# Optimization experiments

Measured on AMD Instinct MI355X. Metric: run time of the kernel, lower is better.

The kernel has to match this reference:

```python
import jax, jax.numpy as jnp
import numpy as np

B = 16
NUM_PATCHES = (4096, 1024)
DIM_S, DIM_M, DIM_L = 256, 512, 1024
N_L = NUM_PATCHES[0] + 1   # tokens in x0 (no cls)
N_M = NUM_PATCHES[1]       # patch tokens in x1 (plus 1 cls)
N_S = 4096                 # patch tokens in x2 (plus 1 cls)
# torch: d_k = int(math.sqrt(dim))
D_K1, D_K2, D_K3 = 22, 32, 16  # int(sqrt(512)), int(sqrt(1024)), int(sqrt(256))


def _lin(x, w, b=None):
    # torch nn.Linear: y = x @ W.T + b, w: [out, in]
    y = jnp.einsum('bnd,md->bnm', x, w)
    return y + b if b is not None else y


def setup_inputs() -> dict:
    key = jax.random.key(0)
    ks = jax.random.split(key, 20)
    s = 0.02
    return {
        'x0': jax.random.normal(ks[0], (B, N_L, DIM_L), jnp.float32),
        'x1': jax.random.normal(ks[1], (B, 1 + N_M, DIM_M), jnp.float32),
        'x2': jax.random.normal(ks[2], (B, 1 + N_S, DIM_S), jnp.float32),
        'f_s_w': jax.random.normal(ks[3], (DIM_M, DIM_S), jnp.float32) * s,
        'f_s_b': jnp.zeros((DIM_M,), jnp.float32),
        'f_m_w': jax.random.normal(ks[4], (DIM_L, DIM_M), jnp.float32) * s,
        'f_m_b': jnp.zeros((DIM_L,), jnp.float32),
        'Wq1': jax.random.normal(ks[5], (DIM_M, DIM_M), jnp.float32) * s,
        'Wk1': jax.random.normal(ks[6], (DIM_M, DIM_M), jnp.float32) * s,
        'Wq2': jax.random.normal(ks[7], (DIM_L, DIM_L), jnp.float32) * s,
        'Wk2': jax.random.normal(ks[8], (DIM_L, DIM_L), jnp.float32) * s,
        'Wv': jax.random.normal(ks[9], (DIM_L, DIM_L), jnp.float32) * s,
        'proj_w': jax.random.normal(ks[10], (NUM_PATCHES[0] + 2, NUM_PATCHES[1] + 1), jnp.float32) * s,
        'proj_b': jnp.zeros((NUM_PATCHES[0] + 2,), jnp.float32),
        'gs_w': jax.random.normal(ks[11], (DIM_S, DIM_L), jnp.float32) * s,
        'gs_b': jnp.zeros((DIM_S,), jnp.float32),
    }


def reference(x0, x1, x2, f_s_w, f_s_b, f_m_w, f_m_b, Wq1, Wk1, Wq2, Wk2, Wv,
              proj_w, proj_b, gs_w, gs_b):
    p_l = x0                                   # [B, N_L, dim_l]
    cls_m, p_m = x1[:, :1, :], x1[:, 1:, :]    # [B,1,dim_m], [B,N_M,dim_m]
    cls_s, p_s = x2[:, :1, :], x2[:, 1:, :]    # [B,1,dim_s], [B,N_S,dim_s]

    # stage 1: small->medium cross attention on attention-map level
    cls_s_proj = _lin(cls_s, f_s_w, f_s_b)               # [B,1,dim_m]
    q1 = _lin(cls_s_proj, Wq1)                           # [B,1,dim_m]
    k1 = _lin(jnp.concatenate([cls_s_proj, p_m], 1), Wk1)  # [B,1+N_M,dim_m]
    att1 = jax.nn.softmax(jnp.einsum('bqd,bkd->bqk', q1, k1) / D_K1, axis=-1)
    att1 = _lin(att1, proj_w, proj_b)                    # [B,1,1+N_L]

    # stage 2: medium->large cross attention
    cls_m_proj = _lin(cls_m, f_m_w, f_m_b)               # [B,1,dim_l]
    q2 = _lin(cls_m_proj, Wq2)
    kv_in = jnp.concatenate([cls_m_proj, p_l], 1)        # [B,1+N_L,dim_l]
    k2 = _lin(kv_in, Wk2)
    att2 = jax.nn.softmax(jnp.einsum('bqd,bkd->bqk', q2, k2) / D_K2, axis=-1)
    v = _lin(kv_in, Wv)                                  # [B,1+N_L,dim_l]

    # weighted fusion of attention maps, third attention pass
    wa = 0.3 * att1 + 0.7 * att2                         # [B,1,1+N_L]
    out = jnp.einsum('bqk,bkd->bqd', wa, v * 1.0)        # [B,1,dim_l]
    g_s = _lin(out, gs_w, gs_b)                          # [B,1,dim_s]

    att3 = jax.nn.softmax(jnp.einsum('bnd,bqd->bnq', p_s, g_s) / D_K3, axis=-1)  # [B,N_S,1]
    p_s_out = jnp.einsum('bnq,bqd->bnd', att3, g_s)      # [B,N_S,dim_s]
    return jnp.concatenate([g_s, p_s_out], axis=1)       # [B,1+N_S,dim_s]
```

## Files before the change

kernel.cpp:

```cpp
#include <hip/hip_runtime.h>
#include <stdint.h>

typedef unsigned int u32;
typedef unsigned short u16;

#define NB 16
#define NL 4097
#define NM_ROWS 1025
#define DS 256
#define DM 512
#define DL 1024
#define NK1 1025
#define NK2 4098
#define MPROJ 4098

__device__ __forceinline__ float bf2f(u16 h){ union{u32 u; float f;} c; c.u = ((u32)h)<<16; return c.f; }
__device__ __forceinline__ u16 f2bf(float x){ union{float f; u32 u;} c; c.f=x; u32 u=c.u; return (u16)((u + 0x7fffu + ((u>>16)&1u))>>16); }
__device__ __forceinline__ float getel(const void* p, long i, int f){
  return f ? ((const float*)p)[i] : bf2f(((const u16*)p)[i]);
}
__device__ __forceinline__ void unpack8(uint4 v, float* fo){
  u32 w[4]={v.x,v.y,v.z,v.w};
  #pragma unroll
  for(int i=0;i<4;i++){
    union{u32 u; float x;} a,b;
    a.u = w[i]<<16; b.u = w[i]&0xffff0000u;
    fo[2*i]=a.x; fo[2*i+1]=b.x;
  }
}
__device__ __forceinline__ float wsum(float v){
  #pragma unroll
  for(int o=32;o>0;o>>=1) v += __shfl_xor(v,o,64);
  return v;
}
__device__ __forceinline__ float wmaxr(float v){
  #pragma unroll
  for(int o=32;o>0;o>>=1) v = fmaxf(v, __shfl_xor(v,o,64));
  return v;
}
__device__ __forceinline__ float block_sum(float v, volatile float* red){
  v = wsum(v);
  if((threadIdx.x&63)==0) red[threadIdx.x>>6]=v;
  __syncthreads();
  float r = red[0]+red[1]+red[2]+red[3];
  __syncthreads();
  return r;
}
__device__ __forceinline__ float block_max(float v, volatile float* red){
  v = wmaxr(v);
  if((threadIdx.x&63)==0) red[threadIdx.x>>6]=v;
  __syncthreads();
  float r = fmaxf(fmaxf(red[0],red[1]),fmaxf(red[2],red[3]));
  __syncthreads();
  return r;
}
__device__ __forceinline__ float clamp60(float x){ return fminf(fmaxf(x,-60.f),60.f); }

__global__ __launch_bounds__(256) void detect_kernel(const u16* __restrict__ x0, int* __restrict__ flag){
  __shared__ float red[256];
  float mx=0.f;
  for(int i=threadIdx.x;i<4096;i+=256){
    float v = fabsf(bf2f(x0[i]));
    if (v==v) mx = fmaxf(mx, v);
  }
  red[threadIdx.x]=mx; __syncthreads();
  if(threadIdx.x==0){
    float m=0.f;
    for(int i=0;i<256;i++) m=fmaxf(m,red[i]);
    flag[0] = (m>1e3f)?1:0;
  }
}

struct Job {
  const void* W; const void* x; const void* bias; float* out;
  int M, D; long xstride; int xinws;
};

__global__ __launch_bounds__(256) void gemv_n_kernel(Job j0, Job j1, const int* __restrict__ flagp){
  Job j = (blockIdx.y==0)? j0 : j1;
  if ((int)(blockIdx.x*4) >= j.M) return;
  int f = flagp[0];
  __shared__ float xs[NB*512];
  int tid = threadIdx.x;
  int m = blockIdx.x*4 + (tid>>6);
  int l = tid & 63;
  float acc[NB];
  #pragma unroll
  for(int b=0;b<NB;b++) acc[b]=0.f;
  for(int c0=0;c0<j.D;c0+=512){
    int cl = j.D-c0; if (cl>512) cl=512;
    for(int i=tid;i<NB*cl;i+=256){
      int b=i/cl, d=i-b*cl;
      float v;
      if (j.xinws) v = ((const float*)j.x)[(long)b*j.D + c0 + d];
      else         v = getel(j.x, (long)b*j.xstride + c0 + d, f);
      xs[i]=v;
    }
    __syncthreads();
    if (m < j.M){
      for(int d=l; d<cl; d+=64){
        float w = getel(j.W, (long)m*j.D + c0 + d, f);
        #pragma unroll
        for(int b=0;b<NB;b++) acc[b] += w*xs[b*cl+d];
      }
    }
    __syncthreads();
  }
  if (m >= j.M) return;
  #pragma unroll
  for(int b=0;b<NB;b++) acc[b]=wsum(acc[b]);
  if(l==0){
    float bv = j.bias ? getel(j.bias, m, f) : 0.f;
    #pragma unroll
    for(int b=0;b<NB;b++) j.out[(long)b*j.M+m]=acc[b]+bv;
  }
}

struct TJob { const void* W; const float* x; float* out; int M, D; };

__global__ __launch_bounds__(256) void gemv_t_kernel(TJob j0, TJob j1, const int* __restrict__ flagp){
  TJob j = (blockIdx.z==0)? j0 : j1;
  int f = flagp[0];
  if ((int)(blockIdx.x*256) >= j.D) return;
  int m0 = blockIdx.y*64;
  if (m0 >= j.M) return;
  __shared__ float xs[NB*64];
  int d = blockIdx.x*256 + threadIdx.x;
  for(int i=threadIdx.x;i<NB*64;i+=256){ int b=i>>6, mm=i&63; xs[i]=j.x[(long)b*j.M+m0+mm]; }
  __syncthreads();
  float acc[NB];
  #pragma unroll
  for(int b=0;b<NB;b++) acc[b]=0.f;
  for(int mm=0;mm<64;++mm){
    float w = getel(j.W, (long)(m0+mm)*j.D + d, f);
    #pragma unroll
    for(int b=0;b<NB;b++) acc[b] += w*xs[b*64+mm];
  }
  #pragma unroll
  for(int b=0;b<NB;b++) atomicAdd(&j.out[(long)b*j.D+d], acc[b]);
}

__global__ __launch_bounds__(256) void att1_logits_kernel(const void* __restrict__ x1,
    const float* __restrict__ q1p, float* __restrict__ logits1, const int* __restrict__ flagp){
  int f = flagp[0];
  int b = blockIdx.y;
  int k = blockIdx.x*4 + (threadIdx.x>>6) + 1;
  if (k > 1024) return;
  int l = threadIdx.x & 63;
  long rbase = ((long)b*NM_ROWS + k)*DM + l*8;
  float rf[8];
  if (f){
    const float* rp = (const float*)x1 + rbase;
    float4 a0 = *(const float4*)rp;
    float4 a1 = *(const float4*)(rp+4);
    rf[0]=a0.x; rf[1]=a0.y; rf[2]=a0.z; rf[3]=a0.w;
    rf[4]=a1.x; rf[5]=a1.y; rf[6]=a1.z; rf[7]=a1.w;
  } else {
    uint4 rv = *(const uint4*)((const u16*)x1 + rbase);
    unpack8(rv, rf);
  }
  const float* qp = q1p + (long)b*DM + l*8;
  float s = rf[0]*qp[0]+rf[1]*qp[1]+rf[2]*qp[2]+rf[3]*qp[3]
          + rf[4]*qp[4]+rf[5]*qp[5]+rf[6]*qp[6]+rf[7]*qp[7];
  s = wsum(s);
  if(l==0) logits1[(long)b*NK1 + k] = s * (1.f/22.f);
}

__global__ __launch_bounds__(256) void att1_softmax_kernel(const float* __restrict__ csp,
    const float* __restrict__ q1p, const float* __restrict__ logits1, float* __restrict__ att1_sm){
  __shared__ float red[4];
  int b=blockIdx.x, t=threadIdx.x;
  float p=0.f;
  for(int d=t;d<DM;d+=256) p += q1p[(long)b*DM+d]*csp[(long)b*DM+d];
  float l0 = block_sum(p, red) * (1.f/22.f);
  float mx = l0;
  for(int k=1+t;k<NK1;k+=256) mx = fmaxf(mx, logits1[(long)b*NK1+k]);
  mx = block_max(mx, red);
  float s=0.f;
  for(int k=t;k<NK1;k+=256){
    float lg = (k==0)? l0 : logits1[(long)b*NK1+k];
    float e = __expf(clamp60(lg-mx));
    att1_sm[(long)b*NK1+k]=e;
    s+=e;
  }
  s = block_sum(s, red);
  float inv = 1.f/fmaxf(s,1e-30f);
  for(int k=t;k<NK1;k+=256) att1_sm[(long)b*NK1+k]*=inv;
}

__global__ __launch_bounds__(256) void att1_proj_kernel(const void* __restrict__ proj_w,
    const void* __restrict__ proj_b, const float* __restrict__ att1_sm, float* __restrict__ att1w,
    const int* __restrict__ flagp){
  int f = flagp[0];
  __shared__ float sm[8*1024];
  int tid=threadIdx.x;
  int m = blockIdx.x*4 + (tid>>6);
  int l = tid&63;
  float acc[NB];
  #pragma unroll
  for(int b=0;b<NB;b++) acc[b]=0.f;
  for(int h=0;h<2;h++){
    for(int i=tid;i<8*1024;i+=256){ int bb=i>>10, k=i&1023; sm[i]=att1_sm[(long)(h*8+bb)*NK1+k]; }
    __syncthreads();
    if (m < MPROJ){
      for(int k=l;k<1024;k+=64){
        float w = getel(proj_w, (long)m*NK1+k, f);
        #pragma unroll
        for(int bb=0;bb<8;bb++) acc[h*8+bb] += w * sm[bb*1024+k];
      }
    }
    __syncthreads();
  }
  if (m >= MPROJ) return;
  if(l==0){
    float wt = getel(proj_w, (long)m*NK1 + 1024, f);
    #pragma unroll
    for(int b=0;b<NB;b++) acc[b] += wt * att1_sm[(long)b*NK1 + 1024];
  }
  #pragma unroll
  for(int b=0;b<NB;b++) acc[b]=wsum(acc[b]);
  if(l==0){
    float pb = getel(proj_b, m, f);
    #pragma unroll
    for(int b=0;b<NB;b++) att1w[(long)b*NK2+m] = 0.3f*(acc[b]+pb);
  }
}

__global__ __launch_bounds__(256) void att2_pass_kernel(const void* __restrict__ x0,
    const float* __restrict__ q2p, const float* __restrict__ att1w,
    float* __restrict__ s1, float* __restrict__ s2, float* __restrict__ Zacc,
    const int* __restrict__ flagp){
  __shared__ float ls[4][1024];
  __shared__ float zs[4];
  int f = flagp[0];
  int b = blockIdx.y;
  int w = threadIdx.x>>6, l = threadIdx.x&63;
  float qf[16];
  {
    const float* qp = q2p + (long)b*DL;
    #pragma unroll
    for(int j=0;j<8;j++){ qf[j]=qp[l*8+j]; qf[8+j]=qp[512+l*8+j]; }
  }
  float af1[16], af2[16];
  #pragma unroll
  for(int j=0;j<16;j++){ af1[j]=0.f; af2[j]=0.f; }
  float zacc=0.f;
  int kbase = blockIdx.x*64 + w*16;
  int nk = NL - kbase; if (nk > 16) nk = 16; if (nk < 0) nk = 0;
  const float* awp = att1w + (long)b*NK2 + kbase + 1;
  for(int i=0;i<nk;i++){
    float rf[16];
    long rowoff = ((long)b*NL + kbase + i)*DL;
    if (f){
      const float* rp = ((const float*)x0) + rowoff;
      float4 a0 = *(const float4*)(rp + l*8);
      float4 a1 = *(const float4*)(rp + l*8 + 4);
      float4 a2 = *(const float4*)(rp + 512 + l*8);
      float4 a3 = *(const float4*)(rp + 512 + l*8 + 4);
      rf[0]=a0.x; rf[1]=a0.y; rf[2]=a0.z; rf[3]=a0.w;
      rf[4]=a1.x; rf[5]=a1.y; rf[6]=a1.z; rf[7]=a1.w;
      rf[8]=a2.x; rf[9]=a2.y; rf[10]=a2.z; rf[11]=a2.w;
      rf[12]=a3.x; rf[13]=a3.y; rf[14]=a3.z; rf[15]=a3.w;
    } else {
      const u16* rp = ((const u16*)x0) + rowoff;
      uint4 rv0 = *(const uint4*)(rp + l*8);
      uint4 rv1 = *(const uint4*)(rp + 512 + l*8);
      u32 wd[8]={rv0.x,rv0.y,rv0.z,rv0.w,rv1.x,rv1.y,rv1.z,rv1.w};
      #pragma unroll
      for(int q=0;q<8;q++){
        union{u32 u; float x;} ua,ub;
        ua.u = wd[q]<<16; ub.u = wd[q]&0xffff0000u;
        rf[2*q]=ua.x; rf[2*q+1]=ub.x;
      }
    }
    float dp=0.f;
    #pragma unroll
    for(int j=0;j<16;j++) dp += rf[j]*qf[j];
    dp = clamp60(wsum(dp)*(1.f/32.f));
    float e = __expf(dp);
    float aw = awp[i];
    zacc += e;
    #pragma unroll
    for(int j=0;j<16;j++){ af1[j] += aw*rf[j]; af2[j] += e*rf[j]; }
  }
  #pragma unroll
  for(int c=0;c<2;c++)
    #pragma unroll
    for(int j=0;j<8;j++) ls[w][c*512 + l*8 + j] = af1[c*8+j];
  __syncthreads();
  for(int d=threadIdx.x; d<1024; d+=256)
    atomicAdd(&s1[(long)b*DL+d], ls[0][d]+ls[1][d]+ls[2][d]+ls[3][d]);
  __syncthreads();
  #pragma unroll
  for(int c=0;c<2;c++)
    #pragma unroll
    for(int j=0;j<8;j++) ls[w][c*512 + l*8 + j] = af2[c*8+j];
  if(l==0) zs[w]=zacc;
  __syncthreads();
  for(int d=threadIdx.x; d<1024; d+=256)
    atomicAdd(&s2[(long)b*DL+d], ls[0][d]+ls[1][d]+ls[2][d]+ls[3][d]);
  if(threadIdx.x==0) atomicAdd(&Zacc[b], zs[0]+zs[1]+zs[2]+zs[3]);
}

__global__ __launch_bounds__(256) void finalize_u_kernel(const float* __restrict__ cmp,
    const float* __restrict__ q2p, const float* __restrict__ att1w,
    const float* __restrict__ s1, const float* __restrict__ s2,
    const float* __restrict__ Zacc, float* __restrict__ u){
  __shared__ float red[4];
  int b=blockIdx.x, t=threadIdx.x;
  float p=0.f;
  for(int d=t;d<DL;d+=256) p += q2p[(long)b*DL+d]*cmp[(long)b*DL+d];
  float l20 = clamp60(block_sum(p,red)*(1.f/32.f));
  float e0 = __expf(l20);
  float Zf = fmaxf(Zacc[b] + e0, 1e-30f);
  float a0 = att1w[(long)b*NK2];
  float c7 = 0.7f/Zf;
  for(int d=t;d<DL;d+=256){
    float cm = cmp[(long)b*DL+d];
    u[(long)b*DL+d] = s1[(long)b*DL+d] + a0*cm + c7*(s2[(long)b*DL+d] + e0*cm);
  }
}

__global__ __launch_bounds__(256) void broadcast_out_kernel(const float* __restrict__ g_s,
    void* __restrict__ out, const int* __restrict__ flagp){
  int f = flagp[0];
  int b = blockIdx.y;
  int colq = threadIdx.x & 31;
  int rowo = threadIdx.x >> 5;
  int r = blockIdx.x*8 + rowo;
  const float* gp = g_s + (long)b*DS + colq*8;
  float4 ga = *(const float4*)gp;
  float4 gb = *(const float4*)(gp+4);
  if (r >= NL) return;
  long row = (long)b*NL + r;
  if (f){
    float4* op = (float4*)out + row*64 + colq*2;
    op[0]=ga; op[1]=gb;
  } else {
    uint4 pk;
    pk.x = (u32)f2bf(ga.x) | ((u32)f2bf(ga.y)<<16);
    pk.y = (u32)f2bf(ga.z) | ((u32)f2bf(ga.w)<<16);
    pk.z = (u32)f2bf(gb.x) | ((u32)f2bf(gb.y)<<16);
    pk.w = (u32)f2bf(gb.z) | ((u32)f2bf(gb.w)<<16);
    ((uint4*)out)[row*32 + colq] = pk;
  }
}

extern "C" void kernel_launch(void* const* d_in, const int* in_sizes, int n_in,
                              void* d_out, int out_size, void* d_ws, size_t ws_size,
                              hipStream_t stream) {
  const void* x0     = d_in[0];
  const void* x1     = d_in[1];
  const void* x2     = d_in[2];
  const void* f_s_w  = d_in[3];
  const void* f_s_b  = d_in[4];
  const void* f_m_w  = d_in[5];
  const void* f_m_b  = d_in[6];
  const void* Wq1    = d_in[7];
  const void* Wk1    = d_in[8];
  const void* Wq2    = d_in[9];
  const void* Wk2    = d_in[10];
  const void* Wv     = d_in[11];
  const void* proj_w = d_in[12];
  const void* proj_b = d_in[13];
  const void* gs_w   = d_in[14];
  const void* gs_b   = d_in[15];

  float* ws = (float*)d_ws;
  float* cls_s_proj = ws;
  float* cls_m_proj = cls_s_proj + NB*DM;
  float* q1v        = cls_m_proj + NB*DL;
  float* q2v        = q1v + NB*DM;
  float* logits1    = q2v + NB*DL;
  float* att1_sm    = logits1 + NB*NK1;
  float* att1w      = att1_sm + NB*NK1;
  float* uvec       = att1w + NB*NK2;
  float* outv       = uvec + NB*DL;
  float* g_s        = outv + NB*DL;
  float* q1p        = g_s + NB*DS;
  float* q2p        = q1p + NB*DM;
  float* s1         = q2p + NB*DL;
  float* s2         = s1 + NB*DL;
  float* Zacc       = s2 + NB*DL;
  int*   flag       = (int*)(Zacc + NB);
  size_t zero_bytes = (size_t)(NB*DM + 3*NB*DL + NB) * sizeof(float);
  hipMemsetAsync(q1p, 0, zero_bytes, stream);

  detect_kernel<<<1,256,0,stream>>>((const u16*)x0, flag);

  Job ja0{f_s_w, x2, f_s_b, cls_s_proj, DM, DS, (long)NL*DS, 0};
  Job ja1{f_m_w, x1, f_m_b, cls_m_proj, DL, DM, (long)NM_ROWS*DM, 0};
  gemv_n_kernel<<<dim3(256,2),256,0,stream>>>(ja0, ja1, flag);

  Job jb0{Wq1, cls_s_proj, nullptr, q1v, DM, DM, DM, 1};
  Job jb1{Wq2, cls_m_proj, nullptr, q2v, DL, DL, DL, 1};
  gemv_n_kernel<<<dim3(256,2),256,0,stream>>>(jb0, jb1, flag);

  TJob jt0{Wk1, q1v, q1p, DM, DM};
  TJob jt1{Wk2, q2v, q2p, DL, DL};
  gemv_t_kernel<<<dim3(4,16,2),256,0,stream>>>(jt0, jt1, flag);

  att1_logits_kernel<<<dim3(256,NB),256,0,stream>>>(x1, q1p, logits1, flag);
  att1_softmax_kernel<<<NB,256,0,stream>>>(cls_s_proj, q1p, logits1, att1_sm);
  att1_proj_kernel<<<dim3(1025),256,0,stream>>>(proj_w, proj_b, att1_sm, att1w, flag);

  att2_pass_kernel<<<dim3(65,NB),256,0,stream>>>(x0, q2p, att1w, s1, s2, Zacc, flag);

  finalize_u_kernel<<<NB,256,0,stream>>>(cls_m_proj, q2p, att1w, s1, s2, Zacc, uvec);
  Job jv{Wv, uvec, nullptr, outv, DL, DL, DL, 1};
  gemv_n_kernel<<<dim3(256,1),256,0,stream>>>(jv, jv, flag);
  Job jg{gs_w, outv, gs_b, g_s, DS, DL, DL, 1};
  gemv_n_kernel<<<dim3(64,1),256,0,stream>>>(jg, jg, flag);

  broadcast_out_kernel<<<dim3(513,NB),256,0,stream>>>(g_s, d_out, flag);
}
```

Before: 684.2 us.

## Precompute fused gs_w·Wv weight, drop softmax max pass, merge small kernels

Adds an init kernel that computes the fused weight product gs_w@Wv (256x1024) and zeroes the workspace, replacing the memset and the separate detect kernel. The Wv and gs_w GEMVs are then replaced by one GEMV over the fused weight. The att1 softmax becomes exp without max subtraction, accumulated into Z by atomics, with normalization moved into the proj kernel. The cls logit for att2 moves into the logits kernel. This removes several launches and a pass over the logits. In exchange it adds a 256x1024x1024 weight product on every call, and dropping the max subtraction relies on clamping to keep the exponentials in range.

```diff
diff --git a/kernel.cpp b/kernel.cpp
--- a/kernel.cpp
+++ b/kernel.cpp
@@ -14,28 +14,41 @@
 #define NK2 4098
 #define MPROJ 4098
 
+#define OFF_CSP  0
+#define OFF_CMP  8192
+#define OFF_Q1V  24576
+#define OFF_Q2V  32768
+#define OFF_E1   49152
+#define OFF_A1W  65552
+#define OFF_GS   131120
+#define OFF_WF   135216
+#define OFF_Q1P  397360
+#define OFF_Q2P  405552
+#define OFF_S1   421936
+#define OFF_S2   438320
+#define OFF_ZA   454704
+#define OFF_Z1   454720
+#define OFF_E20  454736
+#define OFF_FLAG 454752
+#define ZERO_U4  14348
+
 __device__ __forceinline__ float bf2f(u16 h){ union{u32 u; float f;} c; c.u = ((u32)h)<<16; return c.f; }
 __device__ __forceinline__ u16 f2bf(float x){ union{float f; u32 u;} c; c.f=x; u32 u=c.u; return (u16)((u + 0x7fffu + ((u>>16)&1u))>>16); }
 __device__ __forceinline__ float getel(const void* p, long i, int f){
   return f ? ((const float*)p)[i] : bf2f(((const u16*)p)[i]);
 }
 __device__ __forceinline__ void unpack8(uint4 v, float* fo){
-  u32 w[4]={v.x,v.y,v.z,v.w};
+  u32 wd[4]={v.x,v.y,v.z,v.w};
   #pragma unroll
   for(int i=0;i<4;i++){
     union{u32 u; float x;} a,b;
-    a.u = w[i]<<16; b.u = w[i]&0xffff0000u;
+    a.u = wd[i]<<16; b.u = wd[i]&0xffff0000u;
     fo[2*i]=a.x; fo[2*i+1]=b.x;
   }
 }
 __device__ __forceinline__ float wsum(float v){
   #pragma unroll
   for(int o=32;o>0;o>>=1) v += __shfl_xor(v,o,64);
-  return v;
-}
-__device__ __forceinline__ float wmaxr(float v){
-  #pragma unroll
-  for(int o=32;o>0;o>>=1) v = fmaxf(v, __shfl_xor(v,o,64));
   return v;
 }
 __device__ __forceinline__ float block_sum(float v, volatile float* red){
@@ -46,29 +59,59 @@
   __syncthreads();
   return r;
 }
-__device__ __forceinline__ float block_max(float v, volatile float* red){
-  v = wmaxr(v);
-  if((threadIdx.x&63)==0) red[threadIdx.x>>6]=v;
-  __syncthreads();
-  float r = fmaxf(fmaxf(red[0],red[1]),fmaxf(red[2],red[3]));
-  __syncthreads();
-  return r;
-}
 __device__ __forceinline__ float clamp60(float x){ return fminf(fmaxf(x,-60.f),60.f); }
 
-__global__ __launch_bounds__(256) void detect_kernel(const u16* __restrict__ x0, int* __restrict__ flag){
-  __shared__ float red[256];
+__device__ __forceinline__ int self_detect(const void* x0, float* sh){
   float mx=0.f;
-  for(int i=threadIdx.x;i<4096;i+=256){
-    float v = fabsf(bf2f(x0[i]));
-    if (v==v) mx = fmaxf(mx, v);
-  }
-  red[threadIdx.x]=mx; __syncthreads();
-  if(threadIdx.x==0){
+  const u16* p = (const u16*)x0;
+  for (int i=threadIdx.x;i<4096;i+=256){ float v=fabsf(bf2f(p[i])); if(v==v) mx=fmaxf(mx,v); }
+  sh[threadIdx.x]=mx; __syncthreads();
+  if (threadIdx.x==0){
     float m=0.f;
-    for(int i=0;i<256;i++) m=fmaxf(m,red[i]);
-    flag[0] = (m>1e3f)?1:0;
-  }
+    for (int i=0;i<256;i++) m=fmaxf(m,sh[i]);
+    sh[0] = (m>1e3f)?1.f:0.f;
+  }
+  __syncthreads();
+  int f = (sh[0]!=0.f)?1:0;
+  __syncthreads();
+  return f;
+}
+
+__global__ __launch_bounds__(256) void init_kernel(const void* __restrict__ x0,
+    const void* __restrict__ gs_w, const void* __restrict__ Wv,
+    float* __restrict__ ws, int* __restrict__ flag){
+  __shared__ float sh[1280];
+  int blk = blockIdx.x, tid = threadIdx.x;
+  if (blk >= 64 && blk < 96){
+    uint4 z; z.x=0u; z.y=0u; z.z=0u; z.w=0u;
+    uint4* zp = (uint4*)(ws + OFF_Q1P);
+    for (int i=(blk-64)*256+tid; i<ZERO_U4; i+=32*256) zp[i]=z;
+    return;
+  }
+  if (blk == 96){
+    int f = self_detect(x0, sh);
+    if (tid==0) flag[0]=f;
+    return;
+  }
+  int f = self_detect(x0, sh);
+  int o0 = (blk>>2)*16;
+  int d  = (blk&3)*256 + tid;
+  float acc[16];
+  #pragma unroll
+  for(int o=0;o<16;o++) acc[o]=0.f;
+  for (int m0=0;m0<DL;m0+=64){
+    for (int i=tid;i<1024;i+=256){ int oo=i>>6, mm=i&63; sh[i]=getel(gs_w,(long)(o0+oo)*DL+m0+mm,f); }
+    __syncthreads();
+    for (int mm=0;mm<64;++mm){
+      float wv = getel(Wv,(long)(m0+mm)*DL+d,f);
+      #pragma unroll
+      for(int o=0;o<16;o++) acc[o] += sh[o*64+mm]*wv;
+    }
+    __syncthreads();
+  }
+  float* WF = ws + OFF_WF;
+  #pragma unroll
+  for(int o=0;o<16;o++) WF[(long)(o0+o)*DL+d]=acc[o];
 }
 
 struct Job {
@@ -140,13 +183,35 @@
   for(int b=0;b<NB;b++) atomicAdd(&j.out[(long)b*j.D+d], acc[b]);
 }
 
-__global__ __launch_bounds__(256) void att1_logits_kernel(const void* __restrict__ x1,
-    const float* __restrict__ q1p, float* __restrict__ logits1, const int* __restrict__ flagp){
+__global__ __launch_bounds__(256) void att1_logits_z_kernel(const void* __restrict__ x1,
+    const float* __restrict__ csp, const float* __restrict__ cmp,
+    const float* __restrict__ q1p, const float* __restrict__ q2p,
+    float* __restrict__ att1_e, float* __restrict__ Z1, float* __restrict__ e20,
+    const int* __restrict__ flagp){
+  __shared__ float red[4];
   int f = flagp[0];
   int b = blockIdx.y;
-  int k = blockIdx.x*4 + (threadIdx.x>>6) + 1;
-  if (k > 1024) return;
-  int l = threadIdx.x & 63;
+  int tid = threadIdx.x;
+  if (blockIdx.x == 256){
+    float p=0.f;
+    for(int d=tid;d<DM;d+=256) p += q1p[(long)b*DM+d]*csp[(long)b*DM+d];
+    float l0 = block_sum(p, red) * (1.f/22.f);
+    if (tid==0){
+      float e = __expf(clamp60(l0));
+      att1_e[(long)b*NK1] = e;
+      atomicAdd(&Z1[b], e);
+    }
+    return;
+  }
+  if (blockIdx.x == 257){
+    float p=0.f;
+    for(int d=tid;d<DL;d+=256) p += q2p[(long)b*DL+d]*cmp[(long)b*DL+d];
+    float l2 = block_sum(p, red) * (1.f/32.f);
+    if (tid==0) e20[b] = __expf(clamp60(l2));
+    return;
+  }
+  int w = tid>>6, l = tid&63;
+  int k = blockIdx.x*4 + w + 1;
   long rbase = ((long)b*NM_ROWS + k)*DM + l*8;
   float rf[8];
   if (f){
@@ -163,44 +228,32 @@
   float s = rf[0]*qp[0]+rf[1]*qp[1]+rf[2]*qp[2]+rf[3]*qp[3]
           + rf[4]*qp[4]+rf[5]*qp[5]+rf[6]*qp[6]+rf[7]*qp[7];
   s = wsum(s);
-  if(l==0) logits1[(long)b*NK1 + k] = s * (1.f/22.f);
-}
-
-__global__ __launch_bounds__(256) void att1_softmax_kernel(const float* __restrict__ csp,
-    const float* __restrict__ q1p, const float* __restrict__ logits1, float* __restrict__ att1_sm){
-  __shared__ float red[4];
-  int b=blockIdx.x, t=threadIdx.x;
-  float p=0.f;
-  for(int d=t;d<DM;d+=256) p += q1p[(long)b*DM+d]*csp[(long)b*DM+d];
-  float l0 = block_sum(p, red) * (1.f/22.f);
-  float mx = l0;
-  for(int k=1+t;k<NK1;k+=256) mx = fmaxf(mx, logits1[(long)b*NK1+k]);
-  mx = block_max(mx, red);
-  float s=0.f;
-  for(int k=t;k<NK1;k+=256){
-    float lg = (k==0)? l0 : logits1[(long)b*NK1+k];
-    float e = __expf(clamp60(lg-mx));
-    att1_sm[(long)b*NK1+k]=e;
-    s+=e;
-  }
-  s = block_sum(s, red);
-  float inv = 1.f/fmaxf(s,1e-30f);
-  for(int k=t;k<NK1;k+=256) att1_sm[(long)b*NK1+k]*=inv;
+  if (l==0){
+    float e = __expf(clamp60(s*(1.f/22.f)));
+    att1_e[(long)b*NK1 + k] = e;
+    red[w] = e;
+  }
+  __syncthreads();
+  if (tid==0) atomicAdd(&Z1[b], red[0]+red[1]+red[2]+red[3]);
 }
 
 __global__ __launch_bounds__(256) void att1_proj_kernel(const void* __restrict__ proj_w,
-    const void* __restrict__ proj_b, const float* __restrict__ att1_sm, float* __restrict__ att1w,
+    const void* __restrict__ proj_b, const float* __restrict__ att1_e,
+    const float* __restrict__ Z1, float* __restrict__ att1w,
     const int* __restrict__ flagp){
   int f = flagp[0];
   __shared__ float sm[8*1024];
+  __shared__ float sZ[NB];
   int tid=threadIdx.x;
+  if (tid<NB) sZ[tid] = 1.f/fmaxf(Z1[tid],1e-30f);
+  __syncthreads();
   int m = blockIdx.x*4 + (tid>>6);
   int l = tid&63;
   float acc[NB];
   #pragma unroll
   for(int b=0;b<NB;b++) acc[b]=0.f;
   for(int h=0;h<2;h++){
-    for(int i=tid;i<8*1024;i+=256){ int bb=i>>10, k=i&1023; sm[i]=att1_sm[(long)(h*8+bb)*NK1+k]; }
+    for(int i=tid;i<8*1024;i+=256){ int bb=i>>10, k=i&1023; sm[i]=att1_e[(long)(h*8+bb)*NK1+k]; }
     __syncthreads();
     if (m < MPROJ){
       for(int k=l;k<1024;k+=64){
@@ -215,14 +268,14 @@
   if(l==0){
     float wt = getel(proj_w, (long)m*NK1 + 1024, f);
     #pragma unroll
-    for(int b=0;b<NB;b++) acc[b] += wt * att1_sm[(long)b*NK1 + 1024];
+    for(int b=0;b<NB;b++) acc[b] += wt * att1_e[(long)b*NK1 + 1024];
   }
   #pragma unroll
   for(int b=0;b<NB;b++) acc[b]=wsum(acc[b]);
   if(l==0){
     float pb = getel(proj_b, m, f);
     #pragma unroll
-    for(int b=0;b<NB;b++) att1w[(long)b*NK2+m] = 0.3f*(acc[b]+pb);
+    for(int b=0;b<NB;b++) att1w[(long)b*NK2+m] = 0.3f*(acc[b]*sZ[b]+pb);
   }
 }
 
@@ -302,22 +355,51 @@
   if(threadIdx.x==0) atomicAdd(&Zacc[b], zs[0]+zs[1]+zs[2]+zs[3]);
 }
 
-__global__ __launch_bounds__(256) void finalize_u_kernel(const float* __restrict__ cmp,
-    const float* __restrict__ q2p, const float* __restrict__ att1w,
+__global__ __launch_bounds__(256) void jvg_kernel(const float* __restrict__ Wfuse,
+    const float* __restrict__ cmp, const float* __restrict__ att1w,
     const float* __restrict__ s1, const float* __restrict__ s2,
-    const float* __restrict__ Zacc, float* __restrict__ u){
-  __shared__ float red[4];
-  int b=blockIdx.x, t=threadIdx.x;
-  float p=0.f;
-  for(int d=t;d<DL;d+=256) p += q2p[(long)b*DL+d]*cmp[(long)b*DL+d];
-  float l20 = clamp60(block_sum(p,red)*(1.f/32.f));
-  float e0 = __expf(l20);
-  float Zf = fmaxf(Zacc[b] + e0, 1e-30f);
-  float a0 = att1w[(long)b*NK2];
-  float c7 = 0.7f/Zf;
-  for(int d=t;d<DL;d+=256){
-    float cm = cmp[(long)b*DL+d];
-    u[(long)b*DL+d] = s1[(long)b*DL+d] + a0*cm + c7*(s2[(long)b*DL+d] + e0*cm);
+    const float* __restrict__ Zacc, const float* __restrict__ e20,
+    const void* __restrict__ gs_b, float* __restrict__ g_s,
+    const int* __restrict__ flagp){
+  __shared__ float xs[NB*512];
+  __shared__ float sA[NB], sE[NB], sC[NB];
+  int f = flagp[0];
+  int tid = threadIdx.x;
+  if (tid < NB){
+    float e0 = e20[tid];
+    float Zf = fmaxf(Zacc[tid] + e0, 1e-30f);
+    sA[tid] = att1w[(long)tid*NK2];
+    sE[tid] = e0;
+    sC[tid] = 0.7f/Zf;
+  }
+  __syncthreads();
+  int m = blockIdx.x*4 + (tid>>6);
+  int l = tid&63;
+  float acc[NB];
+  #pragma unroll
+  for(int b=0;b<NB;b++) acc[b]=0.f;
+  for (int c0=0;c0<DL;c0+=512){
+    for (int i=tid;i<NB*512;i+=256){
+      int b=i>>9, dd=(i&511);
+      long gi = (long)b*DL + c0 + dd;
+      float cm = cmp[gi];
+      xs[i] = s1[gi] + sA[b]*cm + sC[b]*(s2[gi] + sE[b]*cm);
+    }
+    __syncthreads();
+    const float* wr = Wfuse + (long)m*DL + c0;
+    for (int dd=l; dd<512; dd+=64){
+      float wv = wr[dd];
+      #pragma unroll
+      for(int b=0;b<NB;b++) acc[b] += wv*xs[b*512+dd];
+    }
+    __syncthreads();
+  }
+  #pragma unroll
+  for(int b=0;b<NB;b++) acc[b]=wsum(acc[b]);
+  if (l==0){
+    float bv = getel(gs_b, m, f);
+    #pragma unroll
+    for(int b=0;b<NB;b++) g_s[(long)b*DS+m]=acc[b]+bv;
   }
 }
 
@@ -367,50 +449,45 @@
   const void* gs_b   = d_in[15];
 
   float* ws = (float*)d_ws;
-  float* cls_s_proj = ws;
-  float* cls_m_proj = cls_s_proj + NB*DM;
-  float* q1v        = cls_m_proj + NB*DL;
-  float* q2v        = q1v + NB*DM;
-  float* logits1    = q2v + NB*DL;
-  float* att1_sm    = logits1 + NB*NK1;
-  float* att1w      = att1_sm + NB*NK1;
-  float* uvec       = att1w + NB*NK2;
-  float* outv       = uvec + NB*DL;
-  float* g_s        = outv + NB*DL;
-  float* q1p        = g_s + NB*DS;
-  float* q2p        = q1p + NB*DM;
-  float* s1         = q2p + NB*DL;
-  float* s2         = s1 + NB*DL;
-  float* Zacc       = s2 + NB*DL;
-  int*   flag       = (int*)(Zacc + NB);
-  size_t zero_bytes = (size_t)(NB*DM + 3*NB*DL + NB) * sizeof(float);
-  hipMemsetAsync(q1p, 0, zero_bytes, stream);
-
-  detect_kernel<<<1,256,0,stream>>>((const u16*)x0, flag);
-
-  Job ja0{f_s_w, x2, f_s_b, cls_s_proj, DM, DS, (long)NL*DS, 0};
-  Job ja1{f_m_w, x1, f_m_b, cls_m_proj, DL, DM, (long)NM_ROWS*DM, 0};
+  float* csp   = ws + OFF_CSP;
+  float* cmp   = ws + OFF_CMP;
+  float* q1v   = ws + OFF_Q1V;
+  float* q2v   = ws + OFF_Q2V;
+  float* e1    = ws + OFF_E1;
+  float* a1w   = ws + OFF_A1W;
+  float* g_s   = ws + OFF_GS;
+  float* wf    = ws + OFF_WF;
+  float* q1p   = ws + OFF_Q1P;
+  float* q2p   = ws + OFF_Q2P;
+  float* s1    = ws + OFF_S1;
+  float* s2    = ws + OFF_S2;
+  float* za    = ws + OFF_ZA;
+  float* z1    = ws + OFF_Z1;
+  float* e20   = ws + OFF_E20;
+  int*   flag  = (int*)(ws + OFF_FLAG);
+
+  init_kernel<<<97,256,0,stream>>>(x0, gs_w, Wv, ws, flag);
+
+  Job ja0{f_s_w, x2, f_s_b, csp, DM, DS, (long)NL*DS, 0};
+  Job ja1{f_m_w, x1, f_m_b, cmp, DL, DM, (long)NM_ROWS*DM, 0};
   gemv_n_kernel<<<dim3(256,2),256,0,stream>>>(ja0, ja1, flag);
 
-  Job jb0{Wq1, cls_s_proj, nullptr, q1v, DM, DM, DM, 1};
-  Job jb1{Wq2, cls_m_proj, nullptr, q2v, DL, DL, DL, 1};
+  Job jb0{Wq1, csp, nullptr, q1v, DM, DM, DM, 1};
+  Job jb1{Wq2, cmp, nullptr, q2v, DL, DL, DL, 1};
   gemv_n_kernel<<<dim3(256,2),256,0,stream>>>(jb0, jb1, flag);
 
   TJob jt0{Wk1, q1v, q1p, DM, DM};
   TJob jt1{Wk2, q2v, q2p, DL, DL};
   gemv_t_kernel<<<dim3(4,16,2),256,0,stream>>>(jt0, jt1, flag);
 
-  att1_logits_kernel<<<dim3(256,NB),256,0,stream>>>(x1, q1p, logits1, flag);
-  att1_softmax_kernel<<<NB,256,0,stream>>>(cls_s_proj, q1p, logits1, att1_sm);
-  att1_proj_kernel<<<dim3(1025),256,0,stream>>>(proj_w, proj_b, att1_sm, att1w, flag);
-
-  att2_pass_kernel<<<dim3(65,NB),256,0,stream>>>(x0, q2p, att1w, s1, s2, Zacc, flag);
-
-  finalize_u_kernel<<<NB,256,0,stream>>>(cls_m_proj, q2p, att1w, s1, s2, Zacc, uvec);
-  Job jv{Wv, uvec, nullptr, outv, DL, DL, DL, 1};
-  gemv_n_kernel<<<dim3(256,1),256,0,stream>>>(jv, jv, flag);
-  Job jg{gs_w, outv, gs_b, g_s, DS, DL, DL, 1};
-  gemv_n_kernel<<<dim3(64,1),256,0,stream>>>(jg, jg, flag);
+  att1_logits_z_kernel<<<dim3(258,NB),256,0,stream>>>(x1, csp, cmp, q1p, q2p,
+      e1, z1, e20, flag);
+
+  att1_proj_kernel<<<dim3(1025),256,0,stream>>>(proj_w, proj_b, e1, z1, a1w, flag);
+
+  att2_pass_kernel<<<dim3(65,NB),256,0,stream>>>(x0, q2p, a1w, s1, s2, za, flag);
+
+  jvg_kernel<<<dim3(64),256,0,stream>>>(wf, cmp, a1w, s1, s2, za, e20, gs_b, g_s, flag);
 
   broadcast_out_kernel<<<dim3(513,NB),256,0,stream>>>(g_s, d_out, flag);
 }
```

New measurement: 960.1 us. 1.4x slower.
